# Optimization experiments

Hardware: AMD Instinct MI355X
Metric: run time of the kernel (lower is better)

Reference implementation:

```python
import jax, jax.numpy as jnp
import numpy as np

VOCAB, EMB, ENC = 100000, 256, 256
N_INTENTS, N_SLOTS, LEN_INTENT = 64, 128, 64
B, S = 64, 128


def setup_inputs() -> dict:
    key = jax.random.key(0)
    ks = jax.random.split(key, 8)
    sc = 0.02
    return {
        "token_ids": jax.random.randint(ks[0], (B, S), 0, VOCAB),
        "all_intents": jax.random.randint(ks[1], (B,), 0, N_INTENTS),
        "emb_table": jax.random.normal(ks[2], (VOCAB, EMB), jnp.float32) * sc,
        "doc_enc_W": jax.random.normal(ks[3], (EMB, ENC), jnp.float32) * sc,
        "doc_enc_b": jnp.zeros((ENC,), jnp.float32),
        "slot_enc_W": jax.random.normal(ks[4], (EMB, ENC), jnp.float32) * sc,
        "slot_enc_b": jnp.zeros((ENC,), jnp.float32),
        "doc_dec_W": jax.random.normal(ks[5], (ENC, N_INTENTS), jnp.float32) * sc,
        "doc_dec_b": jnp.zeros((N_INTENTS,), jnp.float32),
        "slot_dec_W": jax.random.normal(ks[6], (ENC + LEN_INTENT, N_SLOTS), jnp.float32) * sc,
        "slot_dec_b": jnp.zeros((N_SLOTS,), jnp.float32),
    }


def reference(token_ids, all_intents, emb_table, doc_enc_W, doc_enc_b,
              slot_enc_W, slot_enc_b, doc_dec_W, doc_dec_b,
              slot_dec_W, slot_dec_b):
    # word embedding lookup: [B, S, EMB] (memory-bound gather)
    emb = emb_table[token_ids]
    # doc encoder: pool sentence then project (batched stand-in for the
    # per-sentence python loop in the original encode())
    sent = jnp.mean(emb, axis=1)                                    # [B, EMB]
    sent_enc = jax.nn.relu(sent @ doc_enc_W + doc_enc_b)            # [B, ENC]
    # intent logits (doc_decoder applied per sentence)
    intent_batch = sent_enc @ doc_dec_W + doc_dec_b                 # [B, N_INTENTS]
    # slot encoder: per-word projection (batched stand-in for per-word loop)
    word_enc = jax.nn.relu(jnp.einsum('bse,eh->bsh', emb, slot_enc_W) + slot_enc_b)
    # use_intent: one-hot of given intent appended to every word encoding
    add_feats = jax.nn.one_hot(all_intents, LEN_INTENT, dtype=word_enc.dtype)  # [B, LEN_INTENT]
    add_feats = jnp.broadcast_to(add_feats[:, None, :], (B, S, LEN_INTENT))
    slot_in = jnp.concatenate([word_enc, add_feats], axis=-1)       # [B, S, ENC+LEN_INTENT]
    slots = jnp.einsum('bsh,ho->bso', slot_in, slot_dec_W) + slot_dec_b
    slots_batch = slots.reshape(B * S, N_SLOTS)  # torch.cat along dim 0 over words
    return intent_batch, slots_batch
```

## Files before the change

kernel.cpp:

```cpp
#include <hip/hip_runtime.h>
#include <hip/hip_bf16.h>

typedef __attribute__((ext_vector_type(8))) short bf16x8;
typedef __attribute__((ext_vector_type(4))) float f32x4;

#define BATCH 64
#define SEQ   128
#define EMB   256
#define ENC   256
#define NIN   64
#define NSL   128

#define W1P_ELEMS (32 * 256 * 8)
#define W2P_ELEMS (32 * 128 * 8)

__global__ __launch_bounds__(256) void prep_kernel(
    const float* __restrict__ slot_enc_W,
    const float* __restrict__ slot_dec_W,
    __hip_bfloat16* __restrict__ w1p,
    __hip_bfloat16* __restrict__ w2p)
{
    const int tid = blockIdx.x * 256 + threadIdx.x;
    if (tid < 8192) {
        const int n  = tid & 255;
        const int bk = tid >> 8;
        union { bf16x8 v; __hip_bfloat16 h[8]; } u;
        #pragma unroll
        for (int j = 0; j < 8; ++j)
            u.h[j] = __float2bfloat16(slot_enc_W[(bk * 8 + j) * ENC + n]);
        *(bf16x8*)(w1p + (size_t)tid * 8) = u.v;
    } else {
        const int t2 = tid - 8192;
        const int n  = t2 & 127;
        const int bk = t2 >> 7;
        union { bf16x8 v; __hip_bfloat16 h[8]; } u;
        #pragma unroll
        for (int j = 0; j < 8; ++j)
            u.h[j] = __float2bfloat16(slot_dec_W[(bk * 8 + j) * NSL + n]);
        *(bf16x8*)(w2p + (size_t)t2 * 8) = u.v;
    }
}

__global__ __launch_bounds__(256) void fused_kernel(
    const int*   __restrict__ token_ids,
    const int*   __restrict__ all_intents,
    const float* __restrict__ emb_table,
    const float* __restrict__ doc_enc_W,
    const float* __restrict__ doc_enc_b,
    const float* __restrict__ slot_enc_b,
    const float* __restrict__ doc_dec_W,
    const float* __restrict__ doc_dec_b,
    const float* __restrict__ slot_dec_W,
    const float* __restrict__ slot_dec_b,
    const __hip_bfloat16* __restrict__ w1p,
    const __hip_bfloat16* __restrict__ w2p,
    float* __restrict__ out_intent,
    float* __restrict__ out_slots)
{
    __shared__ __align__(16) char smem[2 * 16 * 264 * 2];

    const int blk = blockIdx.x;

    if (blk < 512) {
        __hip_bfloat16* lds_emb = (__hip_bfloat16*)smem;
        __hip_bfloat16* lds_we  = (__hip_bfloat16*)(smem + 16 * 264 * 2);

        const int row0 = blk * 16;
        const int wave = threadIdx.x >> 6;
        const int lane = threadIdx.x & 63;
        const int l16  = lane & 15;
        const int quad = lane >> 4;

        #pragma unroll
        for (int i = 0; i < 4; ++i) {
            const int idx = i * 256 + threadIdx.x;
            const int r   = idx >> 6;
            const int c4  = idx & 63;
            const long tok = token_ids[row0 + r];
            const float4 v = *(const float4*)(emb_table + tok * EMB + c4 * 4);
            union { ushort4 s; __hip_bfloat16 h[4]; } u;
            u.h[0] = __float2bfloat16(v.x); u.h[1] = __float2bfloat16(v.y);
            u.h[2] = __float2bfloat16(v.z); u.h[3] = __float2bfloat16(v.w);
            *(ushort4*)(lds_emb + r * 264 + c4 * 4) = u.s;
        }
        __syncthreads();

        f32x4 acc[4];
        #pragma unroll
        for (int nt = 0; nt < 4; ++nt)
            acc[nt] = (f32x4){0.f, 0.f, 0.f, 0.f};

        const int nbase1 = wave * 64;
        #pragma unroll
        for (int ks = 0; ks < 8; ++ks) {
            const bf16x8 a0 = *(const bf16x8*)(lds_emb + l16 * 264 + ks * 32 + quad * 8);
            const int kblk = ks * 4 + quad;
            #pragma unroll
            for (int nt = 0; nt < 4; ++nt) {
                const int n = nbase1 + nt * 16 + l16;
                const bf16x8 bf = *(const bf16x8*)(w1p + ((size_t)kblk * 256 + n) * 8);
                acc[nt] = __builtin_amdgcn_mfma_f32_16x16x32_bf16(a0, bf, acc[nt], 0, 0, 0);
            }
        }

        #pragma unroll
        for (int nt = 0; nt < 4; ++nt) {
            const int col = nbase1 + nt * 16 + l16;
            const float bias = slot_enc_b[col];
            #pragma unroll
            for (int r = 0; r < 4; ++r) {
                const int row = quad * 4 + r;
                lds_we[row * 264 + col] =
                    __float2bfloat16(fmaxf(acc[nt][r] + bias, 0.f));
            }
        }
        __syncthreads();

        f32x4 acc2[2];
        #pragma unroll
        for (int nt = 0; nt < 2; ++nt)
            acc2[nt] = (f32x4){0.f, 0.f, 0.f, 0.f};

        const int nbase2 = wave * 32;
        #pragma unroll
        for (int ks = 0; ks < 8; ++ks) {
            const bf16x8 a0 = *(const bf16x8*)(lds_we + l16 * 264 + ks * 32 + quad * 8);
            const int kblk = ks * 4 + quad;
            #pragma unroll
            for (int nt = 0; nt < 2; ++nt) {
                const int n = nbase2 + nt * 16 + l16;
                const bf16x8 bf = *(const bf16x8*)(w2p + ((size_t)kblk * 128 + n) * 8);
                acc2[nt] = __builtin_amdgcn_mfma_f32_16x16x32_bf16(a0, bf, acc2[nt], 0, 0, 0);
            }
        }

        const int intent = all_intents[blk >> 3];
        const float* hotrow = slot_dec_W + (long)(256 + intent) * NSL;

        #pragma unroll
        for (int nt = 0; nt < 2; ++nt) {
            const int col = nbase2 + nt * 16 + l16;
            const float add = slot_dec_b[col] + hotrow[col];
            #pragma unroll
            for (int r = 0; r < 4; ++r) {
                const int row = quad * 4 + r;
                out_slots[(long)(row0 + row) * NSL + col] = acc2[nt][r] + add;
            }
        }
    } else {
        float* red  = (float*)smem;
        float* sent = (float*)(smem + 4096);
        float* senc = (float*)(smem + 4096 + 1024);

        const int b  = blk - 512;
        const int t  = threadIdx.x;
        const int wv = t >> 6;
        const int ln = t & 63;
        const int* toks = token_ids + b * SEQ;

        float4 accv = make_float4(0.f, 0.f, 0.f, 0.f);
        #pragma unroll 8
        for (int i = 0; i < 32; ++i) {
            const long tok = toks[wv * 32 + i];
            const float4 v = *(const float4*)(emb_table + tok * EMB + ln * 4);
            accv.x += v.x; accv.y += v.y; accv.z += v.z; accv.w += v.w;
        }
        *(float4*)(&red[wv * 256 + ln * 4]) = accv;
        __syncthreads();

        sent[t] = (red[0 * 256 + t] + red[1 * 256 + t] +
                   red[2 * 256 + t] + red[3 * 256 + t]) * (1.0f / 128.0f);
        __syncthreads();

        float a = doc_enc_b[t];
        #pragma unroll 16
        for (int k = 0; k < EMB; ++k)
            a = fmaf(sent[k], doc_enc_W[k * ENC + t], a);
        senc[t] = fmaxf(a, 0.f);
        __syncthreads();

        if (t < NIN) {
            float a2 = doc_dec_b[t];
            #pragma unroll 16
            for (int k = 0; k < ENC; ++k)
                a2 = fmaf(senc[k], doc_dec_W[k * NIN + t], a2);
            out_intent[b * NIN + t] = a2;
        }
    }
}

extern "C" void kernel_launch(void* const* d_in, const int* in_sizes, int n_in,
                              void* d_out, int out_size, void* d_ws, size_t ws_size,
                              hipStream_t stream) {
    const int*   token_ids   = (const int*)d_in[0];
    const int*   all_intents = (const int*)d_in[1];
    const float* emb_table   = (const float*)d_in[2];
    const float* doc_enc_W   = (const float*)d_in[3];
    const float* doc_enc_b   = (const float*)d_in[4];
    const float* slot_enc_W  = (const float*)d_in[5];
    const float* slot_enc_b  = (const float*)d_in[6];
    const float* doc_dec_W   = (const float*)d_in[7];
    const float* doc_dec_b   = (const float*)d_in[8];
    const float* slot_dec_W  = (const float*)d_in[9];
    const float* slot_dec_b  = (const float*)d_in[10];

    __hip_bfloat16* w1p = (__hip_bfloat16*)d_ws;
    __hip_bfloat16* w2p = w1p + W1P_ELEMS;

    float* out = (float*)d_out;

    prep_kernel<<<48, 256, 0, stream>>>(slot_enc_W, slot_dec_W, w1p, w2p);

    fused_kernel<<<576, 256, 0, stream>>>(
        token_ids, all_intents, emb_table, doc_enc_W, doc_enc_b,
        slot_enc_b, doc_dec_W, doc_dec_b, slot_dec_W, slot_dec_b,
        w1p, w2p,
        out, out + BATCH * NIN);
}
```

Measured before the change: 169.5 us.

## Compute doc encoder/decoder with bf16 MFMA and fold into slot blocks

Pre-packs the doc encoder and decoder weights to bf16 in the prep kernel and computes the sentence projection and intent logits with MFMA instead of scalar FMA loops. These doc computations no longer run in 64 dedicated tail blocks: every eighth slot block (the first block of each batch) does its batch's intent work before its own slot tile, giving a 512-block grid. The aim is to remove the slow serial per-thread FMA loops over fp32 weights and the tail blocks. The cost is that 64 blocks carry extra latency, the prep kernel does more work, and intent logits lose precision from bf16 rounding.

```diff
diff --git a/kernel.cpp b/kernel.cpp
--- a/kernel.cpp
+++ b/kernel.cpp
@@ -11,180 +11,214 @@
 #define NIN   64
 #define NSL   128
 
-#define W1P_ELEMS (32 * 256 * 8)
-#define W2P_ELEMS (32 * 128 * 8)
+#define W1P_OFF   0
+#define W2P_OFF   65536
+#define DW1P_OFF  98304
+#define DW2P_OFF  163840
+
+#define PACK(W, NCOLS, DST, IDX) {                                            \
+    const int n  = (IDX) & ((NCOLS) - 1);                                     \
+    const int bk = (IDX) / (NCOLS);                                           \
+    union { bf16x8 v; __hip_bfloat16 h[8]; } u;                               \
+    _Pragma("unroll")                                                         \
+    for (int j = 0; j < 8; ++j)                                               \
+        u.h[j] = __float2bfloat16((W)[(bk * 8 + j) * (NCOLS) + n]);           \
+    *(bf16x8*)((DST) + (size_t)(IDX) * 8) = u.v; }
 
 __global__ __launch_bounds__(256) void prep_kernel(
     const float* __restrict__ slot_enc_W,
     const float* __restrict__ slot_dec_W,
-    __hip_bfloat16* __restrict__ w1p,
-    __hip_bfloat16* __restrict__ w2p)
+    const float* __restrict__ doc_enc_W,
+    const float* __restrict__ doc_dec_W,
+    __hip_bfloat16* __restrict__ ws)
 {
     const int tid = blockIdx.x * 256 + threadIdx.x;
     if (tid < 8192) {
-        const int n  = tid & 255;
-        const int bk = tid >> 8;
-        union { bf16x8 v; __hip_bfloat16 h[8]; } u;
-        #pragma unroll
-        for (int j = 0; j < 8; ++j)
-            u.h[j] = __float2bfloat16(slot_enc_W[(bk * 8 + j) * ENC + n]);
-        *(bf16x8*)(w1p + (size_t)tid * 8) = u.v;
+        PACK(slot_enc_W, 256, ws + W1P_OFF,  tid);
+    } else if (tid < 12288) {
+        PACK(slot_dec_W, 128, ws + W2P_OFF,  tid - 8192);
+    } else if (tid < 20480) {
+        PACK(doc_enc_W,  256, ws + DW1P_OFF, tid - 12288);
     } else {
-        const int t2 = tid - 8192;
-        const int n  = t2 & 127;
-        const int bk = t2 >> 7;
-        union { bf16x8 v; __hip_bfloat16 h[8]; } u;
-        #pragma unroll
-        for (int j = 0; j < 8; ++j)
-            u.h[j] = __float2bfloat16(slot_dec_W[(bk * 8 + j) * NSL + n]);
-        *(bf16x8*)(w2p + (size_t)t2 * 8) = u.v;
-    }
+        PACK(doc_dec_W,   64, ws + DW2P_OFF, tid - 20480);
+    }
+}
+
+static __device__ __forceinline__ bf16x8 cvt8(const float4 lo, const float4 hi) {
+    union { bf16x8 v; __hip_bfloat16 h[8]; } u;
+    u.h[0] = __float2bfloat16(lo.x); u.h[1] = __float2bfloat16(lo.y);
+    u.h[2] = __float2bfloat16(lo.z); u.h[3] = __float2bfloat16(lo.w);
+    u.h[4] = __float2bfloat16(hi.x); u.h[5] = __float2bfloat16(hi.y);
+    u.h[6] = __float2bfloat16(hi.z); u.h[7] = __float2bfloat16(hi.w);
+    return u.v;
 }
 
 __global__ __launch_bounds__(256) void fused_kernel(
     const int*   __restrict__ token_ids,
     const int*   __restrict__ all_intents,
     const float* __restrict__ emb_table,
-    const float* __restrict__ doc_enc_W,
     const float* __restrict__ doc_enc_b,
     const float* __restrict__ slot_enc_b,
-    const float* __restrict__ doc_dec_W,
     const float* __restrict__ doc_dec_b,
     const float* __restrict__ slot_dec_W,
     const float* __restrict__ slot_dec_b,
-    const __hip_bfloat16* __restrict__ w1p,
-    const __hip_bfloat16* __restrict__ w2p,
+    const __hip_bfloat16* __restrict__ ws,
     float* __restrict__ out_intent,
     float* __restrict__ out_slots)
 {
     __shared__ __align__(16) char smem[2 * 16 * 264 * 2];
 
-    const int blk = blockIdx.x;
-
-    if (blk < 512) {
-        __hip_bfloat16* lds_emb = (__hip_bfloat16*)smem;
-        __hip_bfloat16* lds_we  = (__hip_bfloat16*)(smem + 16 * 264 * 2);
-
-        const int row0 = blk * 16;
-        const int wave = threadIdx.x >> 6;
-        const int lane = threadIdx.x & 63;
-        const int l16  = lane & 15;
-        const int quad = lane >> 4;
-
-        #pragma unroll
-        for (int i = 0; i < 4; ++i) {
-            const int idx = i * 256 + threadIdx.x;
-            const int r   = idx >> 6;
-            const int c4  = idx & 63;
-            const long tok = token_ids[row0 + r];
-            const float4 v = *(const float4*)(emb_table + tok * EMB + c4 * 4);
-            union { ushort4 s; __hip_bfloat16 h[4]; } u;
-            u.h[0] = __float2bfloat16(v.x); u.h[1] = __float2bfloat16(v.y);
-            u.h[2] = __float2bfloat16(v.z); u.h[3] = __float2bfloat16(v.w);
-            *(ushort4*)(lds_emb + r * 264 + c4 * 4) = u.s;
-        }
-        __syncthreads();
-
-        f32x4 acc[4];
-        #pragma unroll
-        for (int nt = 0; nt < 4; ++nt)
-            acc[nt] = (f32x4){0.f, 0.f, 0.f, 0.f};
-
-        const int nbase1 = wave * 64;
+    const int blk  = blockIdx.x;
+    const int wave = threadIdx.x >> 6;
+    const int lane = threadIdx.x & 63;
+    const int l16  = lane & 15;
+    const int quad = lane >> 4;
+
+    const __hip_bfloat16* w1p  = ws + W1P_OFF;
+    const __hip_bfloat16* w2p  = ws + W2P_OFF;
+    const __hip_bfloat16* dw1p = ws + DW1P_OFF;
+    const __hip_bfloat16* dw2p = ws + DW2P_OFF;
+
+    if ((blk & 7) == 0) {
+        float* red  = (float*)smem;
+        float* sent = (float*)(smem + 4096);
+        float* senc = (float*)(smem + 5120);
+
+        const int b  = blk >> 3;
+        const int t  = threadIdx.x;
+        const int* toks = token_ids + b * SEQ;
+
+        float4 accv = make_float4(0.f, 0.f, 0.f, 0.f);
+        #pragma unroll 8
+        for (int i = 0; i < 32; ++i) {
+            const long tok = toks[wave * 32 + i];
+            const float4 v = *(const float4*)(emb_table + tok * EMB + lane * 4);
+            accv.x += v.x; accv.y += v.y; accv.z += v.z; accv.w += v.w;
+        }
+        *(float4*)(&red[wave * 256 + lane * 4]) = accv;
+        __syncthreads();
+
+        sent[t] = (red[t] + red[256 + t] + red[512 + t] + red[768 + t])
+                  * (1.0f / 128.0f);
+        __syncthreads();
+
+        f32x4 dacc[4];
+        #pragma unroll
+        for (int nt = 0; nt < 4; ++nt) dacc[nt] = (f32x4){0.f, 0.f, 0.f, 0.f};
+
         #pragma unroll
         for (int ks = 0; ks < 8; ++ks) {
-            const bf16x8 a0 = *(const bf16x8*)(lds_emb + l16 * 264 + ks * 32 + quad * 8);
+            const float* sp = sent + ks * 32 + quad * 8;
+            const bf16x8 a = cvt8(*(const float4*)sp, *(const float4*)(sp + 4));
             const int kblk = ks * 4 + quad;
             #pragma unroll
             for (int nt = 0; nt < 4; ++nt) {
-                const int n = nbase1 + nt * 16 + l16;
-                const bf16x8 bf = *(const bf16x8*)(w1p + ((size_t)kblk * 256 + n) * 8);
-                acc[nt] = __builtin_amdgcn_mfma_f32_16x16x32_bf16(a0, bf, acc[nt], 0, 0, 0);
+                const int n = wave * 64 + nt * 16 + l16;
+                const bf16x8 bf = *(const bf16x8*)(dw1p + ((size_t)kblk * 256 + n) * 8);
+                dacc[nt] = __builtin_amdgcn_mfma_f32_16x16x32_bf16(a, bf, dacc[nt], 0, 0, 0);
             }
         }
-
+        if (quad == 0) {
+            #pragma unroll
+            for (int nt = 0; nt < 4; ++nt) {
+                const int col = wave * 64 + nt * 16 + l16;
+                senc[col] = fmaxf(dacc[nt][0] + doc_enc_b[col], 0.f);
+            }
+        }
+        __syncthreads();
+
+        f32x4 iacc = (f32x4){0.f, 0.f, 0.f, 0.f};
+        #pragma unroll
+        for (int ks = 0; ks < 8; ++ks) {
+            const float* sp = senc + ks * 32 + quad * 8;
+            const bf16x8 a = cvt8(*(const float4*)sp, *(const float4*)(sp + 4));
+            const int kblk = ks * 4 + quad;
+            const int n = wave * 16 + l16;
+            const bf16x8 bf = *(const bf16x8*)(dw2p + ((size_t)kblk * 64 + n) * 8);
+            iacc = __builtin_amdgcn_mfma_f32_16x16x32_bf16(a, bf, iacc, 0, 0, 0);
+        }
+        if (quad == 0)
+            out_intent[b * NIN + wave * 16 + l16] = iacc[0] + doc_dec_b[wave * 16 + l16];
+        __syncthreads();
+    }
+
+    __hip_bfloat16* lds_emb = (__hip_bfloat16*)smem;
+    __hip_bfloat16* lds_we  = (__hip_bfloat16*)(smem + 16 * 264 * 2);
+
+    const int row0 = blk * 16;
+
+    #pragma unroll
+    for (int i = 0; i < 4; ++i) {
+        const int idx = i * 256 + threadIdx.x;
+        const int r   = idx >> 6;
+        const int c4  = idx & 63;
+        const long tok = token_ids[row0 + r];
+        const float4 v = *(const float4*)(emb_table + tok * EMB + c4 * 4);
+        union { ushort4 s; __hip_bfloat16 h[4]; } u;
+        u.h[0] = __float2bfloat16(v.x); u.h[1] = __float2bfloat16(v.y);
+        u.h[2] = __float2bfloat16(v.z); u.h[3] = __float2bfloat16(v.w);
+        *(ushort4*)(lds_emb + r * 264 + c4 * 4) = u.s;
+    }
+    __syncthreads();
+
+    f32x4 acc[4];
+    #pragma unroll
+    for (int nt = 0; nt < 4; ++nt) acc[nt] = (f32x4){0.f, 0.f, 0.f, 0.f};
+
+    const int nbase1 = wave * 64;
+    #pragma unroll
+    for (int ks = 0; ks < 8; ++ks) {
+        const bf16x8 a0 = *(const bf16x8*)(lds_emb + l16 * 264 + ks * 32 + quad * 8);
+        const int kblk = ks * 4 + quad;
         #pragma unroll
         for (int nt = 0; nt < 4; ++nt) {
-            const int col = nbase1 + nt * 16 + l16;
-            const float bias = slot_enc_b[col];
-            #pragma unroll
-            for (int r = 0; r < 4; ++r) {
-                const int row = quad * 4 + r;
-                lds_we[row * 264 + col] =
-                    __float2bfloat16(fmaxf(acc[nt][r] + bias, 0.f));
-            }
-        }
-        __syncthreads();
-
-        f32x4 acc2[2];
-        #pragma unroll
-        for (int nt = 0; nt < 2; ++nt)
-            acc2[nt] = (f32x4){0.f, 0.f, 0.f, 0.f};
-
-        const int nbase2 = wave * 32;
-        #pragma unroll
-        for (int ks = 0; ks < 8; ++ks) {
-            const bf16x8 a0 = *(const bf16x8*)(lds_we + l16 * 264 + ks * 32 + quad * 8);
-            const int kblk = ks * 4 + quad;
-            #pragma unroll
-            for (int nt = 0; nt < 2; ++nt) {
-                const int n = nbase2 + nt * 16 + l16;
-                const bf16x8 bf = *(const bf16x8*)(w2p + ((size_t)kblk * 128 + n) * 8);
-                acc2[nt] = __builtin_amdgcn_mfma_f32_16x16x32_bf16(a0, bf, acc2[nt], 0, 0, 0);
-            }
-        }
-
-        const int intent = all_intents[blk >> 3];
-        const float* hotrow = slot_dec_W + (long)(256 + intent) * NSL;
-
+            const int n = nbase1 + nt * 16 + l16;
+            const bf16x8 bf = *(const bf16x8*)(w1p + ((size_t)kblk * 256 + n) * 8);
+            acc[nt] = __builtin_amdgcn_mfma_f32_16x16x32_bf16(a0, bf, acc[nt], 0, 0, 0);
+        }
+    }
+
+    #pragma unroll
+    for (int nt = 0; nt < 4; ++nt) {
+        const int col = nbase1 + nt * 16 + l16;
+        const float bias = slot_enc_b[col];
+        #pragma unroll
+        for (int r = 0; r < 4; ++r) {
+            const int row = quad * 4 + r;
+            lds_we[row * 264 + col] =
+                __float2bfloat16(fmaxf(acc[nt][r] + bias, 0.f));
+        }
+    }
+    __syncthreads();
+
+    f32x4 acc2[2];
+    #pragma unroll
+    for (int nt = 0; nt < 2; ++nt) acc2[nt] = (f32x4){0.f, 0.f, 0.f, 0.f};
+
+    const int nbase2 = wave * 32;
+    #pragma unroll
+    for (int ks = 0; ks < 8; ++ks) {
+        const bf16x8 a0 = *(const bf16x8*)(lds_we + l16 * 264 + ks * 32 + quad * 8);
+        const int kblk = ks * 4 + quad;
         #pragma unroll
         for (int nt = 0; nt < 2; ++nt) {
-            const int col = nbase2 + nt * 16 + l16;
-            const float add = slot_dec_b[col] + hotrow[col];
-            #pragma unroll
-            for (int r = 0; r < 4; ++r) {
-                const int row = quad * 4 + r;
-                out_slots[(long)(row0 + row) * NSL + col] = acc2[nt][r] + add;
-            }
-        }
-    } else {
-        float* red  = (float*)smem;
-        float* sent = (float*)(smem + 4096);
-        float* senc = (float*)(smem + 4096 + 1024);
-
-        const int b  = blk - 512;
-        const int t  = threadIdx.x;
-        const int wv = t >> 6;
-        const int ln = t & 63;
-        const int* toks = token_ids + b * SEQ;
-
-        float4 accv = make_float4(0.f, 0.f, 0.f, 0.f);
-        #pragma unroll 8
-        for (int i = 0; i < 32; ++i) {
-            const long tok = toks[wv * 32 + i];
-            const float4 v = *(const float4*)(emb_table + tok * EMB + ln * 4);
-            accv.x += v.x; accv.y += v.y; accv.z += v.z; accv.w += v.w;
-        }
-        *(float4*)(&red[wv * 256 + ln * 4]) = accv;
-        __syncthreads();
-
-        sent[t] = (red[0 * 256 + t] + red[1 * 256 + t] +
-                   red[2 * 256 + t] + red[3 * 256 + t]) * (1.0f / 128.0f);
-        __syncthreads();
-
-        float a = doc_enc_b[t];
-        #pragma unroll 16
-        for (int k = 0; k < EMB; ++k)
-            a = fmaf(sent[k], doc_enc_W[k * ENC + t], a);
-        senc[t] = fmaxf(a, 0.f);
-        __syncthreads();
-
-        if (t < NIN) {
-            float a2 = doc_dec_b[t];
-            #pragma unroll 16
-            for (int k = 0; k < ENC; ++k)
-                a2 = fmaf(senc[k], doc_dec_W[k * NIN + t], a2);
-            out_intent[b * NIN + t] = a2;
+            const int n = nbase2 + nt * 16 + l16;
+            const bf16x8 bf = *(const bf16x8*)(w2p + ((size_t)kblk * 128 + n) * 8);
+            acc2[nt] = __builtin_amdgcn_mfma_f32_16x16x32_bf16(a0, bf, acc2[nt], 0, 0, 0);
+        }
+    }
+
+    const int intent = all_intents[blk >> 3];
+    const float* hotrow = slot_dec_W + (long)(256 + intent) * NSL;
+
+    #pragma unroll
+    for (int nt = 0; nt < 2; ++nt) {
+        const int col = nbase2 + nt * 16 + l16;
+        const float add = slot_dec_b[col] + hotrow[col];
+        #pragma unroll
+        for (int r = 0; r < 4; ++r) {
+            const int row = quad * 4 + r;
+            out_slots[(long)(row0 + row) * NSL + col] = acc2[nt][r] + add;
         }
     }
 }
@@ -204,16 +238,14 @@
     const float* slot_dec_W  = (const float*)d_in[9];
     const float* slot_dec_b  = (const float*)d_in[10];
 
-    __hip_bfloat16* w1p = (__hip_bfloat16*)d_ws;
-    __hip_bfloat16* w2p = w1p + W1P_ELEMS;
-
+    __hip_bfloat16* ws = (__hip_bfloat16*)d_ws;
     float* out = (float*)d_out;
 
-    prep_kernel<<<48, 256, 0, stream>>>(slot_enc_W, slot_dec_W, w1p, w2p);
-
-    fused_kernel<<<576, 256, 0, stream>>>(
-        token_ids, all_intents, emb_table, doc_enc_W, doc_enc_b,
-        slot_enc_b, doc_dec_W, doc_dec_b, slot_dec_W, slot_dec_b,
-        w1p, w2p,
-        out, out + BATCH * NIN);
-}
+    prep_kernel<<<88, 256, 0, stream>>>(slot_enc_W, slot_dec_W,
+                                        doc_enc_W, doc_dec_W, ws);
+
+    fused_kernel<<<512, 256, 0, stream>>>(
+        token_ids, all_intents, emb_table, doc_enc_b,
+        slot_enc_b, doc_dec_b, slot_dec_W, slot_dec_b,
+        ws, out, out + BATCH * NIN);
+}
```

After: 164.0 us. -3.3%, faster.
